# Kernel optimization log

Measured on AMD Instinct MI355X. Metric: run time of the kernel, lower is better.

Reference implementation:

```python
import jax, jax.numpy as jnp
import numpy as np

ROWS, COLS, H, W = 128, 128, 128, 128
B, C = 2, 16
DENSITY = 0.01  # classic Hough vote matrix is very sparse binary


def setup_inputs() -> dict:
    key = jax.random.key(0)
    k_img, k_vote = jax.random.split(key)
    image = jax.random.normal(k_img, (B, C, ROWS, COLS), dtype=jnp.float32)
    # sparse binary voting matrix, shape (rows, cols, h, w)
    vote_index = (jax.random.uniform(k_vote, (ROWS, COLS, H, W)) < DENSITY).astype(jnp.float32)
    return {"image": image, "vote_index": vote_index}


def reference(image, vote_index):
    rows, cols, h, w = vote_index.shape
    b, c = image.shape[0], image.shape[1]
    V = vote_index.reshape(rows * cols, h * w)          # (rows*cols, h*w)
    x = jax.nn.relu(image.reshape(b * c, rows * cols))  # (b*c, rows*cols)
    ht = (x @ V) / cols                                 # (b*c, h*w)
    return ht.reshape(b, c, h, w)
```

## Files before the change

### kernel.cpp

```cpp
#include <hip/hip_runtime.h>

constexpr int Mdim = 32;
constexpr int Kdim = 16384;
constexpr int Ndim = 16384;

constexpr int TPB = 256;

constexpr int KT     = 8;
constexpr int KC     = Kdim / KT;
constexpr int SLABS  = KC / 32;
constexpr int NT32   = Ndim / 32;
constexpr int NWAVES = NT32 * KT;
constexpr int NBLK   = NWAVES / 4;

typedef short bf16x8 __attribute__((ext_vector_type(8)));
typedef float f32x4  __attribute__((ext_vector_type(4)));

__device__ __forceinline__ short f32_to_bf16(float f) {
    union { float f; unsigned u; } c; c.f = f;
    unsigned u = c.u;
    u += 0x7fffu + ((u >> 16) & 1u);
    return (short)(u >> 16);
}

__global__ __launch_bounds__(TPB)
void build_xa(const float* __restrict__ image, short* __restrict__ xa) {
    const int g    = blockIdx.x * TPB + threadIdx.x;
    const int lane = g & 63;
    const int frag = g >> 6;
    const int mt   = frag & 1;
    const int kc   = frag >> 1;
    const int m    = mt * 16 + (lane & 15);
    const int k    = kc * 32 + (lane >> 4) * 8;
    const float* src = image + (size_t)m * Kdim + k;

    bf16x8 o;
    #pragma unroll
    for (int j = 0; j < 8; ++j)
        o[j] = f32_to_bf16(fmaxf(src[j], 0.0f) * (1.0f / 128.0f));
    reinterpret_cast<bf16x8*>(xa)[g] = o;
}

__global__ __launch_bounds__(TPB, 4)
void ht_gemm(const short* __restrict__ xa,
             const float* __restrict__ vote,
             float* __restrict__ parts)
{
    const int tid  = threadIdx.x;
    const int lane = tid & 63;
    const int w    = tid >> 6;
    const int wv   = blockIdx.x * 4 + w;
    const int nt   = wv & (NT32 - 1);
    const int kch  = wv >> 9;
    const int k0   = kch * KC;

    const int bq   = lane >> 4;
    const int bn   = lane & 15;
    const int ncol = nt * 32 + bn;

    f32x4 acc[2][2];
    #pragma unroll
    for (int a = 0; a < 2; ++a)
        #pragma unroll
        for (int b = 0; b < 2; ++b) { f32x4 z = {0.f, 0.f, 0.f, 0.f}; acc[a][b] = z; }

    const float* vbase = vote + (size_t)(k0 + bq * 8) * Ndim + ncol;
    const short* abase = xa + ((size_t)(k0 >> 5) * 128 + lane) * 8;

    float b0[16], b1[16];

    auto load_b = [&](float* d, int s) {
        const float* p = vbase + (size_t)s * 32 * Ndim;
        #pragma unroll
        for (int j = 0; j < 8; ++j) {
            d[j]     = p[(size_t)j * Ndim];
            d[8 + j] = p[(size_t)j * Ndim + 16];
        }
    };
    auto compute = [&](const float* b, int s) {
        const bf16x8 a0 = *reinterpret_cast<const bf16x8*>(abase + (size_t)s * 1024);
        const bf16x8 a1 = *reinterpret_cast<const bf16x8*>(abase + (size_t)s * 1024 + 512);
        bf16x8 f0, f1;
        #pragma unroll
        for (int j = 0; j < 8; ++j) {
            f0[j] = f32_to_bf16(b[j]);
            f1[j] = f32_to_bf16(b[8 + j]);
        }
        acc[0][0] = __builtin_amdgcn_mfma_f32_16x16x32_bf16(a0, f0, acc[0][0], 0, 0, 0);
        acc[1][0] = __builtin_amdgcn_mfma_f32_16x16x32_bf16(a1, f0, acc[1][0], 0, 0, 0);
        acc[0][1] = __builtin_amdgcn_mfma_f32_16x16x32_bf16(a0, f1, acc[0][1], 0, 0, 0);
        acc[1][1] = __builtin_amdgcn_mfma_f32_16x16x32_bf16(a1, f1, acc[1][1], 0, 0, 0);
    };

    load_b(b0, 0);
    for (int s = 0; s < SLABS; s += 2) {
        load_b(b1, s + 1);
        compute(b0, s);
        if (s + 2 < SLABS) load_b(b0, s + 2);
        compute(b1, s + 1);
    }

    float* pb = parts + (size_t)kch * ((size_t)Mdim * Ndim);
    #pragma unroll
    for (int mt = 0; mt < 2; ++mt)
        #pragma unroll
        for (int cl = 0; cl < 2; ++cl)
            #pragma unroll
            for (int r = 0; r < 4; ++r) {
                const int row = mt * 16 + bq * 4 + r;
                const int col = nt * 32 + cl * 16 + bn;
                pb[(size_t)row * Ndim + col] = acc[mt][cl][r];
            }
}

__global__ __launch_bounds__(TPB)
void ht_reduce(const float* __restrict__ parts, float* __restrict__ out, int nchunks) {
    const size_t i4 = (size_t)blockIdx.x * TPB + threadIdx.x;
    const float4* p = reinterpret_cast<const float4*>(parts) + i4;
    float4 s = make_float4(0.f, 0.f, 0.f, 0.f);
    constexpr size_t stride4 = (size_t)Mdim * Ndim / 4;
    for (int c = 0; c < nchunks; ++c) {
        const float4 v = p[(size_t)c * stride4];
        s.x += v.x; s.y += v.y; s.z += v.z; s.w += v.w;
    }
    reinterpret_cast<float4*>(out)[i4] = s;
}

__global__ __launch_bounds__(TPB)
void ht_gemm_atomic(const float* __restrict__ image, const float* __restrict__ vote,
                    float* __restrict__ out) {
    __shared__ float xsh[256 * Mdim];
    const int tid = threadIdx.x;
    const int ntile = blockIdx.x % 16;
    const int k0 = (blockIdx.x / 16) * 256;
    const int nn0 = ntile * 1024 + tid * 4;
    for (int idx = tid; idx < 256 * Mdim; idx += TPB) {
        const int kk = idx >> 5, m = idx & 31;
        xsh[idx] = fmaxf(image[(size_t)m * Kdim + (k0 + kk)], 0.0f) * (1.0f / 128.0f);
    }
    __syncthreads();
    float4 acc[Mdim];
    #pragma unroll
    for (int m = 0; m < Mdim; ++m) acc[m] = make_float4(0.f, 0.f, 0.f, 0.f);
    const float* vptr = vote + (size_t)k0 * Ndim + nn0;
    for (int kk = 0; kk < 256; ++kk) {
        const float4 v = *reinterpret_cast<const float4*>(vptr);
        vptr += Ndim;
        #pragma unroll
        for (int m = 0; m < Mdim; ++m) {
            const float s = xsh[kk * Mdim + m];
            acc[m].x = fmaf(s, v.x, acc[m].x); acc[m].y = fmaf(s, v.y, acc[m].y);
            acc[m].z = fmaf(s, v.z, acc[m].z); acc[m].w = fmaf(s, v.w, acc[m].w);
        }
    }
    #pragma unroll
    for (int m = 0; m < Mdim; ++m) {
        float* o = out + (size_t)m * Ndim + nn0;
        unsafeAtomicAdd(o + 0, acc[m].x); unsafeAtomicAdd(o + 1, acc[m].y);
        unsafeAtomicAdd(o + 2, acc[m].z); unsafeAtomicAdd(o + 3, acc[m].w);
    }
}

extern "C" void kernel_launch(void* const* d_in, const int* in_sizes, int n_in,
                              void* d_out, int out_size, void* d_ws, size_t ws_size,
                              hipStream_t stream) {
    const float* image = (const float*)d_in[0];
    const float* vote  = (const float*)d_in[1];
    float* out = (float*)d_out;

    const size_t xa_bytes    = (size_t)(Kdim / 32) * 2 * 64 * 8 * sizeof(short);
    const size_t chunk_bytes = (size_t)Mdim * Ndim * sizeof(float);

    if (xa_bytes + (size_t)KT * chunk_bytes > ws_size) {
        (void)hipMemsetAsync(out, 0, (size_t)out_size * sizeof(float), stream);
        ht_gemm_atomic<<<dim3(16 * 64), TPB, 0, stream>>>(image, vote, out);
        return;
    }

    short* xa    = (short*)d_ws;
    float* parts = (float*)((char*)d_ws + xa_bytes);

    build_xa<<<dim3((Kdim / 32) * 2 * 64 / TPB), TPB, 0, stream>>>(image, xa);
    ht_gemm<<<dim3(NBLK), TPB, 0, stream>>>(xa, vote, parts);
    ht_reduce<<<dim3((Mdim * Ndim) / (4 * TPB)), TPB, 0, stream>>>(parts, out, KT);
}
```

Baseline: 1.328 ms.

## Switch to 32x32x16 bf16 MFMA with a four-deep nontemporal load pipeline

```diff
diff --git a/kernel.cpp b/kernel.cpp
--- a/kernel.cpp
+++ b/kernel.cpp
@@ -8,13 +8,13 @@
 
 constexpr int KT     = 8;
 constexpr int KC     = Kdim / KT;
-constexpr int SLABS  = KC / 32;
+constexpr int SLABS  = KC / 16;
 constexpr int NT32   = Ndim / 32;
-constexpr int NWAVES = NT32 * KT;
-constexpr int NBLK   = NWAVES / 4;
+constexpr int NBLK   = NT32 * KT / 4;
+constexpr int DEPTH  = 4;
 
 typedef short bf16x8 __attribute__((ext_vector_type(8)));
-typedef float f32x4  __attribute__((ext_vector_type(4)));
+typedef float f32x16 __attribute__((ext_vector_type(16)));
 
 __device__ __forceinline__ short f32_to_bf16(float f) {
     union { float f; unsigned u; } c; c.f = f;
@@ -27,11 +27,9 @@
 void build_xa(const float* __restrict__ image, short* __restrict__ xa) {
     const int g    = blockIdx.x * TPB + threadIdx.x;
     const int lane = g & 63;
-    const int frag = g >> 6;
-    const int mt   = frag & 1;
-    const int kc   = frag >> 1;
-    const int m    = mt * 16 + (lane & 15);
-    const int k    = kc * 32 + (lane >> 4) * 8;
+    const int slab = g >> 6;
+    const int m    = lane & 31;
+    const int k    = slab * 16 + (lane >> 5) * 8;
     const float* src = image + (size_t)m * Kdim + k;
 
     bf16x8 o;
@@ -54,63 +52,50 @@
     const int kch  = wv >> 9;
     const int k0   = kch * KC;
 
-    const int bq   = lane >> 4;
-    const int bn   = lane & 15;
-    const int ncol = nt * 32 + bn;
+    const int col  = nt * 32 + (lane & 31);
+    const int krow = (lane >> 5) * 8;
 
-    f32x4 acc[2][2];
+    const float* vbase = vote + (size_t)(k0 + krow) * Ndim + col;
+    const short* abase = xa + ((size_t)(k0 / 16) * 64 + lane) * 8;
+
+    f32x16 acc;
     #pragma unroll
-    for (int a = 0; a < 2; ++a)
+    for (int i = 0; i < 16; ++i) acc[i] = 0.0f;
+
+    float  bv[DEPTH][8];
+    bf16x8 av[DEPTH];
+
+    auto load = [&](int slot, int s) {
+        const float* p = vbase + (size_t)s * 16 * Ndim;
         #pragma unroll
-        for (int b = 0; b < 2; ++b) { f32x4 z = {0.f, 0.f, 0.f, 0.f}; acc[a][b] = z; }
-
-    const float* vbase = vote + (size_t)(k0 + bq * 8) * Ndim + ncol;
-    const short* abase = xa + ((size_t)(k0 >> 5) * 128 + lane) * 8;
-
-    float b0[16], b1[16];
-
-    auto load_b = [&](float* d, int s) {
-        const float* p = vbase + (size_t)s * 32 * Ndim;
+        for (int j = 0; j < 8; ++j)
+            bv[slot][j] = __builtin_nontemporal_load(p + (size_t)j * Ndim);
+        av[slot] = *reinterpret_cast<const bf16x8*>(abase + (size_t)s * 512);
+    };
+    auto comp = [&](int slot) {
+        bf16x8 f;
         #pragma unroll
-        for (int j = 0; j < 8; ++j) {
-            d[j]     = p[(size_t)j * Ndim];
-            d[8 + j] = p[(size_t)j * Ndim + 16];
-        }
-    };
-    auto compute = [&](const float* b, int s) {
-        const bf16x8 a0 = *reinterpret_cast<const bf16x8*>(abase + (size_t)s * 1024);
-        const bf16x8 a1 = *reinterpret_cast<const bf16x8*>(abase + (size_t)s * 1024 + 512);
-        bf16x8 f0, f1;
-        #pragma unroll
-        for (int j = 0; j < 8; ++j) {
-            f0[j] = f32_to_bf16(b[j]);
-            f1[j] = f32_to_bf16(b[8 + j]);
-        }
-        acc[0][0] = __builtin_amdgcn_mfma_f32_16x16x32_bf16(a0, f0, acc[0][0], 0, 0, 0);
-        acc[1][0] = __builtin_amdgcn_mfma_f32_16x16x32_bf16(a1, f0, acc[1][0], 0, 0, 0);
-        acc[0][1] = __builtin_amdgcn_mfma_f32_16x16x32_bf16(a0, f1, acc[0][1], 0, 0, 0);
-        acc[1][1] = __builtin_amdgcn_mfma_f32_16x16x32_bf16(a1, f1, acc[1][1], 0, 0, 0);
+        for (int j = 0; j < 8; ++j) f[j] = f32_to_bf16(bv[slot][j]);
+        acc = __builtin_amdgcn_mfma_f32_32x32x16_bf16(av[slot], f, acc, 0, 0, 0);
     };
 
-    load_b(b0, 0);
-    for (int s = 0; s < SLABS; s += 2) {
-        load_b(b1, s + 1);
-        compute(b0, s);
-        if (s + 2 < SLABS) load_b(b0, s + 2);
-        compute(b1, s + 1);
+    #pragma unroll
+    for (int u = 0; u < DEPTH; ++u) load(u, u);
+    for (int s = 0; s < SLABS; s += DEPTH) {
+        #pragma unroll
+        for (int u = 0; u < DEPTH; ++u) {
+            comp(u);
+            if (s + DEPTH + u < SLABS) load(u, s + DEPTH + u);
+        }
     }
 
     float* pb = parts + (size_t)kch * ((size_t)Mdim * Ndim);
+    const int rbase = 4 * (lane >> 5);
     #pragma unroll
-    for (int mt = 0; mt < 2; ++mt)
-        #pragma unroll
-        for (int cl = 0; cl < 2; ++cl)
-            #pragma unroll
-            for (int r = 0; r < 4; ++r) {
-                const int row = mt * 16 + bq * 4 + r;
-                const int col = nt * 32 + cl * 16 + bn;
-                pb[(size_t)row * Ndim + col] = acc[mt][cl][r];
-            }
+    for (int r = 0; r < 16; ++r) {
+        const int row = (r & 3) + 8 * (r >> 2) + rbase;
+        pb[(size_t)row * Ndim + col] = acc[r];
+    }
 }
 
 __global__ __launch_bounds__(TPB)
@@ -168,7 +153,7 @@
     const float* vote  = (const float*)d_in[1];
     float* out = (float*)d_out;
 
-    const size_t xa_bytes    = (size_t)(Kdim / 32) * 2 * 64 * 8 * sizeof(short);
+    const size_t xa_bytes    = (size_t)(Kdim / 16) * 64 * 8 * sizeof(short);
     const size_t chunk_bytes = (size_t)Mdim * Ndim * sizeof(float);
 
     if (xa_bytes + (size_t)KT * chunk_bytes > ws_size) {
@@ -180,7 +165,7 @@
     short* xa    = (short*)d_ws;
     float* parts = (float*)((char*)d_ws + xa_bytes);
 
-    build_xa<<<dim3((Kdim / 32) * 2 * 64 / TPB), TPB, 0, stream>>>(image, xa);
+    build_xa<<<dim3((Kdim / 16) * 64 / TPB), TPB, 0, stream>>>(image, xa);
     ht_gemm<<<dim3(NBLK), TPB, 0, stream>>>(xa, vote, parts);
     ht_reduce<<<dim3((Mdim * Ndim) / (4 * TPB)), TPB, 0, stream>>>(parts, out, KT);
 }
```

Result: faster. 1.298 ms, median of 2 (-2.3%).
